# Kernel tuning notes

Hardware: AMD Instinct MI355X
Metric: run time of the kernel (lower is better)

## Reference

```python
import jax, jax.numpy as jnp
import numpy as np

B = 4096
D_FULL, D_T1, D_T2 = 1024, 512, 512
N_SPEC, N_SHARED = 4, 4
HID, OUT = 512, 256


def _expert_params(key, n_experts, d_in):
    k1, k2, k3, k4 = jax.random.split(key, 4)
    s1 = 1.0 / np.sqrt(d_in)
    s2 = 1.0 / np.sqrt(HID)
    return {
        'W1': jax.random.uniform(k1, (n_experts, d_in, HID), jnp.float32, -s1, s1),
        'b1': jax.random.uniform(k2, (n_experts, HID), jnp.float32, -s1, s1),
        'W2': jax.random.uniform(k3, (n_experts, HID, OUT), jnp.float32, -s2, s2),
        'b2': jax.random.uniform(k4, (n_experts, OUT), jnp.float32, -s2, s2),
    }


def setup_inputs() -> dict:
    key = jax.random.key(0)
    ks = jax.random.split(key, 12)
    x_full = jax.random.normal(ks[0], (B, D_FULL), jnp.float32)
    x_task1 = jax.random.normal(ks[1], (B, D_T1), jnp.float32)
    x_task2 = jax.random.normal(ks[2], (B, D_T2), jnp.float32)
    ps = _expert_params(ks[3], N_SHARED, D_FULL)
    p1 = _expert_params(ks[4], N_SPEC, D_T1)
    p2 = _expert_params(ks[5], N_SPEC, D_T2)
    sg = 1.0 / np.sqrt(D_FULL)
    s1 = 1.0 / np.sqrt(D_T1)
    s2 = 1.0 / np.sqrt(D_T2)
    return {
        'x_full': x_full, 'x_task1': x_task1, 'x_task2': x_task2,
        'sh_W1': ps['W1'], 'sh_b1': ps['b1'], 'sh_W2': ps['W2'], 'sh_b2': ps['b2'],
        't1_W1': p1['W1'], 't1_b1': p1['b1'], 't1_W2': p1['W2'], 't1_b2': p1['b2'],
        't2_W1': p2['W1'], 't2_b1': p2['b1'], 't2_W2': p2['W2'], 't2_b2': p2['b2'],
        'gsh_W': jax.random.uniform(ks[6], (D_FULL, 2 * N_SPEC + N_SHARED), jnp.float32, -sg, sg),
        'gsh_b': jax.random.uniform(ks[7], (2 * N_SPEC + N_SHARED,), jnp.float32, -sg, sg),
        'g1_W': jax.random.uniform(ks[8], (D_T1, N_SPEC + N_SHARED), jnp.float32, -s1, s1),
        'g1_b': jax.random.uniform(ks[9], (N_SPEC + N_SHARED,), jnp.float32, -s1, s1),
        'g2_W': jax.random.uniform(ks[10], (D_T2, N_SPEC + N_SHARED), jnp.float32, -s2, s2),
        'g2_b': jax.random.uniform(ks[11], (N_SPEC + N_SHARED,), jnp.float32, -s2, s2),
    }


def _experts(x, W1, b1, W2, b2):
    # x: [B, D]; W1: [E, D, H] -> out [E, B, OUT]
    h = jax.nn.relu(jnp.einsum('bd,edh->ebh', x, W1) + b1[:, None, :])
    return jax.nn.relu(jnp.einsum('ebh,eho->ebo', h, W2) + b2[:, None, :])


def reference(x_full, x_task1, x_task2,
              sh_W1, sh_b1, sh_W2, sh_b2,
              t1_W1, t1_b1, t1_W2, t1_b2,
              t2_W1, t2_b1, t2_W2, t2_b2,
              gsh_W, gsh_b, g1_W, g1_b, g2_W, g2_b):
    eo_shared = _experts(x_full, sh_W1, sh_b1, sh_W2, sh_b2)    # [Es, B, OUT]
    eo_t1 = _experts(x_task1, t1_W1, t1_b1, t1_W2, t1_b2)       # [Et, B, OUT]
    eo_t2 = _experts(x_task2, t2_W1, t2_b1, t2_W2, t2_b2)       # [Et, B, OUT]

    g1 = jax.nn.softmax(x_task1 @ g1_W + g1_b, axis=1)          # [B, Et+Es]
    out1 = jnp.einsum('ebc,be->bc', jnp.concatenate([eo_t1, eo_shared], axis=0), g1)

    g2 = jax.nn.softmax(x_task2 @ g2_W + g2_b, axis=1)
    out2 = jnp.einsum('ebc,be->bc', jnp.concatenate([eo_t2, eo_shared], axis=0), g2)

    gsh = jax.nn.softmax(x_full @ gsh_W + gsh_b, axis=1)        # [B, 2Et+Es]
    out_sh = jnp.einsum('ebc,be->bc', jnp.concatenate([eo_t1, eo_t2, eo_shared], axis=0), gsh)

    return (out_sh, out1, out2)
```

## Files before the change

kernel.cpp:

```cpp
#include <hip/hip_runtime.h>

typedef unsigned short u16;
typedef __attribute__((ext_vector_type(8))) short short8;
typedef __attribute__((ext_vector_type(4))) float f32x4;

#define GL2LDS16(src, dst) __builtin_amdgcn_global_load_lds( \
    (const __attribute__((address_space(1))) void*)(src),    \
    (__attribute__((address_space(3))) void*)(dst), 16, 0, 0)

__device__ __forceinline__ u16 f2bf(float f) {
  union { float f; unsigned u; } v; v.f = f;
  unsigned r = v.u + 0x7fffu + ((v.u >> 16) & 1u);
  return (u16)(r >> 16);
}
__device__ __forceinline__ float bf2f(u16 h) {
  union { unsigned u; float f; } v; v.u = ((unsigned)h) << 16; return v.f;
}

__global__ void k_cvt_bf16(const float* __restrict__ in, u16* __restrict__ out, int n8) {
  int i = blockIdx.x * 256 + threadIdx.x;
  if (i >= n8) return;
  const float4* p = (const float4*)in + 2 * (size_t)i;
  float4 a = p[0], b = p[1];
  short8 o;
  o[0] = (short)f2bf(a.x); o[1] = (short)f2bf(a.y); o[2] = (short)f2bf(a.z); o[3] = (short)f2bf(a.w);
  o[4] = (short)f2bf(b.x); o[5] = (short)f2bf(b.y); o[6] = (short)f2bf(b.z); o[7] = (short)f2bf(b.w);
  ((short8*)out)[i] = o;
}

__global__ void k_transpose_cvt(const float* __restrict__ in, u16* __restrict__ out, int R, int C) {
  __shared__ float tile[32][33];
  size_t zoff = (size_t)blockIdx.z * R * C;
  in += zoff; out += zoff;
  int c0 = blockIdx.x * 32, r0 = blockIdx.y * 32;
  int tx = threadIdx.x, ty = threadIdx.y;
#pragma unroll
  for (int i = ty; i < 32; i += 8)
    tile[i][tx] = in[(size_t)(r0 + i) * C + (c0 + tx)];
  __syncthreads();
#pragma unroll
  for (int i = ty; i < 32; i += 8)
    out[(size_t)(c0 + i) * R + (r0 + tx)] = f2bf(tile[tx][i]);
}

template <int NG, int KD>
__device__ __forceinline__ void gate_row(const float* __restrict__ x, const float* __restrict__ W,
                                         const float* __restrict__ bv, float* __restrict__ out,
                                         int b, int lane) {
  float s[NG];
#pragma unroll
  for (int j = 0; j < NG; ++j) s[j] = 0.f;
  const float* xr = x + (size_t)b * KD;
  for (int k = lane; k < KD; k += 64) {
    float xv = xr[k];
    const float* wr = W + (size_t)k * NG;
#pragma unroll
    for (int j = 0; j < NG; ++j) s[j] += xv * wr[j];
  }
#pragma unroll
  for (int off = 32; off >= 1; off >>= 1) {
#pragma unroll
    for (int j = 0; j < NG; ++j) s[j] += __shfl_xor(s[j], off, 64);
  }
#pragma unroll
  for (int j = 0; j < NG; ++j) s[j] += bv[j];
  float m = s[0];
#pragma unroll
  for (int j = 1; j < NG; ++j) m = fmaxf(m, s[j]);
  float tot = 0.f;
#pragma unroll
  for (int j = 0; j < NG; ++j) { s[j] = __expf(s[j] - m); tot += s[j]; }
  float inv = 1.f / tot;
  if (lane == 0) {
#pragma unroll
    for (int j = 0; j < NG; ++j) out[(size_t)b * NG + j] = s[j] * inv;
  }
}

__global__ void k_gates(const float* __restrict__ xf, const float* __restrict__ x1,
                        const float* __restrict__ x2,
                        const float* __restrict__ gshW, const float* __restrict__ gshB,
                        const float* __restrict__ g1W, const float* __restrict__ g1B,
                        const float* __restrict__ g2W, const float* __restrict__ g2B,
                        float* __restrict__ gsh, float* __restrict__ g1, float* __restrict__ g2) {
  int b = blockIdx.x, lane = threadIdx.x;
  gate_row<12, 1024>(xf, gshW, gshB, gsh, b, lane);
  gate_row<8, 512>(x1, g1W, g1B, g1, b, lane);
  gate_row<8, 512>(x2, g2W, g2B, g2, b, lane);
}

struct GemmDesc {
  const u16* A;
  const u16* BT;
  const float* bias;
  u16* C;
  int K;
  int N;
};
struct GemmArgs { GemmDesc d[12]; };

__global__ __launch_bounds__(256, 2) void k_gemm(GemmArgs args) {
  GemmDesc g = args.d[blockIdx.y];
  const int K = g.K, N = g.N;
  const int row0 = (blockIdx.x & 31) << 7;
  const int col0 = (blockIdx.x >> 5) << 7;

  __shared__ __align__(16) u16 As[128 * 32];
  __shared__ __align__(16) u16 Bs[128 * 32];

  const int lane = threadIdx.x & 63;
  const int wave = threadIdx.x >> 6;
  const int wr = (wave >> 1) << 6;
  const int wc = (wave & 1) << 6;
  const int lrow = lane & 15;
  const int kgrp = (lane >> 4) << 3;

  f32x4 acc[4][4];
#pragma unroll
  for (int m = 0; m < 4; ++m)
#pragma unroll
    for (int n = 0; n < 4; ++n)
      acc[m][n] = (f32x4){0.f, 0.f, 0.f, 0.f};

  for (int k0 = 0; k0 < K; k0 += 32) {
#pragma unroll
    for (int i = 0; i < 2; ++i) {
      const int cb = (i * 4 + wave) * 64;
      const int c = cb + lane;
      const int r = c >> 2;
      const int kk = (c & 3) << 3;
      GL2LDS16(g.A + (size_t)(row0 + r) * K + (k0 + kk), &As[cb * 8]);
      GL2LDS16(g.BT + (size_t)(col0 + r) * K + (k0 + kk), &Bs[cb * 8]);
    }
    __syncthreads();

    short8 a[4], b[4];
#pragma unroll
    for (int m = 0; m < 4; ++m)
      a[m] = *(const short8*)&As[(wr + (m << 4) + lrow) * 32 + kgrp];
#pragma unroll
    for (int n = 0; n < 4; ++n)
      b[n] = *(const short8*)&Bs[(wc + (n << 4) + lrow) * 32 + kgrp];
#pragma unroll
    for (int m = 0; m < 4; ++m)
#pragma unroll
      for (int n = 0; n < 4; ++n)
        acc[m][n] = __builtin_amdgcn_mfma_f32_16x16x32_bf16(a[m], b[n], acc[m][n], 0, 0, 0);
    __syncthreads();
  }

  const int rbase = (lane >> 4) << 2;
#pragma unroll
  for (int n = 0; n < 4; ++n) {
    const int gc = col0 + wc + (n << 4) + lrow;
    const float bv = g.bias[gc];
#pragma unroll
    for (int m = 0; m < 4; ++m) {
      const int gr = row0 + wr + (m << 4) + rbase;
#pragma unroll
      for (int j = 0; j < 4; ++j) {
        float o = acc[m][n][j] + bv;
        o = fmaxf(o, 0.f);
        g.C[(size_t)(gr + j) * N + gc] = f2bf(o);
      }
    }
  }
}

__global__ void k_reduce(const u16* __restrict__ OutB, const float* __restrict__ gsh,
                         const float* __restrict__ g1, const float* __restrict__ g2,
                         float* __restrict__ out) {
  int t = blockIdx.x * 256 + threadIdx.x;
  int b = t >> 5;
  int c0 = (t & 31) << 3;
  float wsh[12], w1[8], w2[8];
#pragma unroll
  for (int j = 0; j < 12; ++j) wsh[j] = gsh[(size_t)b * 12 + j];
#pragma unroll
  for (int j = 0; j < 8; ++j) { w1[j] = g1[(size_t)b * 8 + j]; w2[j] = g2[(size_t)b * 8 + j]; }
  float ash[8] = {0, 0, 0, 0, 0, 0, 0, 0};
  float a1[8] = {0, 0, 0, 0, 0, 0, 0, 0};
  float a2[8] = {0, 0, 0, 0, 0, 0, 0, 0};
#pragma unroll
  for (int e = 0; e < 12; ++e) {
    short8 v = *(const short8*)&OutB[((size_t)e * 4096 + b) * 256 + c0];
    float f[8];
#pragma unroll
    for (int i = 0; i < 8; ++i) f[i] = bf2f((u16)v[i]);
#pragma unroll
    for (int i = 0; i < 8; ++i) ash[i] += wsh[e] * f[i];
    if (e < 4) {
#pragma unroll
      for (int i = 0; i < 8; ++i) a1[i] += w1[e] * f[i];
    } else if (e < 8) {
#pragma unroll
      for (int i = 0; i < 8; ++i) a2[i] += w2[e - 4] * f[i];
    } else {
#pragma unroll
      for (int i = 0; i < 8; ++i) a1[i] += w1[e - 4] * f[i];
#pragma unroll
      for (int i = 0; i < 8; ++i) a2[i] += w2[e - 4] * f[i];
    }
  }
  size_t base = (size_t)b * 256 + c0;
  float4* o;
  o = (float4*)(out + base);
  o[0] = make_float4(ash[0], ash[1], ash[2], ash[3]);
  o[1] = make_float4(ash[4], ash[5], ash[6], ash[7]);
  o = (float4*)(out + 4096ull * 256 + base);
  o[0] = make_float4(a1[0], a1[1], a1[2], a1[3]);
  o[1] = make_float4(a1[4], a1[5], a1[6], a1[7]);
  o = (float4*)(out + 2ull * 4096 * 256 + base);
  o[0] = make_float4(a2[0], a2[1], a2[2], a2[3]);
  o[1] = make_float4(a2[4], a2[5], a2[6], a2[7]);
}

extern "C" void kernel_launch(void* const* d_in, const int* in_sizes, int n_in,
                              void* d_out, int out_size, void* d_ws, size_t ws_size,
                              hipStream_t stream) {
  const float* x_full = (const float*)d_in[0];
  const float* x_t1 = (const float*)d_in[1];
  const float* x_t2 = (const float*)d_in[2];
  const float* sh_W1 = (const float*)d_in[3];
  const float* sh_b1 = (const float*)d_in[4];
  const float* sh_W2 = (const float*)d_in[5];
  const float* sh_b2 = (const float*)d_in[6];
  const float* t1_W1 = (const float*)d_in[7];
  const float* t1_b1 = (const float*)d_in[8];
  const float* t1_W2 = (const float*)d_in[9];
  const float* t1_b2 = (const float*)d_in[10];
  const float* t2_W1 = (const float*)d_in[11];
  const float* t2_b1 = (const float*)d_in[12];
  const float* t2_W2 = (const float*)d_in[13];
  const float* t2_b2 = (const float*)d_in[14];
  const float* gsh_W = (const float*)d_in[15];
  const float* gsh_b = (const float*)d_in[16];
  const float* g1_W = (const float*)d_in[17];
  const float* g1_b = (const float*)d_in[18];
  const float* g2_W = (const float*)d_in[19];
  const float* g2_b = (const float*)d_in[20];

  char* ws = (char*)d_ws;
  size_t off = 0;
  auto alloc = [&](size_t bytes) -> void* {
    void* p = ws + off;
    off += (bytes + 255) & ~(size_t)255;
    return p;
  };
  u16* xf_b = (u16*)alloc(4096ull * 1024 * 2);
  u16* x1_b = (u16*)alloc(4096ull * 512 * 2);
  u16* x2_b = (u16*)alloc(4096ull * 512 * 2);
  u16* w1t_t1 = (u16*)alloc(4ull * 512 * 512 * 2);
  u16* w1t_t2 = (u16*)alloc(4ull * 512 * 512 * 2);
  u16* w1t_sh = (u16*)alloc(4ull * 512 * 1024 * 2);
  u16* w2t = (u16*)alloc(12ull * 256 * 512 * 2);
  u16* H = (u16*)alloc(12ull * 4096 * 512 * 2);
  u16* OutB = (u16*)alloc(12ull * 4096 * 256 * 2);
  float* gshv = (float*)alloc(4096ull * 12 * 4);
  float* g1v = (float*)alloc(4096ull * 8 * 4);
  float* g2v = (float*)alloc(4096ull * 8 * 4);

  k_cvt_bf16<<<4096 * 1024 / 8 / 256, 256, 0, stream>>>(x_full, xf_b, 4096 * 1024 / 8);
  k_cvt_bf16<<<4096 * 512 / 8 / 256, 256, 0, stream>>>(x_t1, x1_b, 4096 * 512 / 8);
  k_cvt_bf16<<<4096 * 512 / 8 / 256, 256, 0, stream>>>(x_t2, x2_b, 4096 * 512 / 8);

  k_transpose_cvt<<<dim3(16, 16, 4), dim3(32, 8), 0, stream>>>(t1_W1, w1t_t1, 512, 512);
  k_transpose_cvt<<<dim3(16, 16, 4), dim3(32, 8), 0, stream>>>(t2_W1, w1t_t2, 512, 512);
  k_transpose_cvt<<<dim3(16, 32, 4), dim3(32, 8), 0, stream>>>(sh_W1, w1t_sh, 1024, 512);
  k_transpose_cvt<<<dim3(8, 16, 4), dim3(32, 8), 0, stream>>>(t1_W2, w2t, 512, 256);
  k_transpose_cvt<<<dim3(8, 16, 4), dim3(32, 8), 0, stream>>>(t2_W2, w2t + 4ull * 256 * 512, 512, 256);
  k_transpose_cvt<<<dim3(8, 16, 4), dim3(32, 8), 0, stream>>>(sh_W2, w2t + 8ull * 256 * 512, 512, 256);

  k_gates<<<4096, 64, 0, stream>>>(x_full, x_t1, x_t2, gsh_W, gsh_b, g1_W, g1_b, g2_W, g2_b,
                                   gshv, g1v, g2v);

  GemmArgs ga1;
  for (int e = 0; e < 4; ++e) {
    ga1.d[e] = GemmDesc{xf_b, w1t_sh + (size_t)e * 512 * 1024, sh_b1 + e * 512,
                        H + (size_t)(8 + e) * 4096 * 512, 1024, 512};
    ga1.d[4 + e] = GemmDesc{x1_b, w1t_t1 + (size_t)e * 512 * 512, t1_b1 + e * 512,
                            H + (size_t)e * 4096 * 512, 512, 512};
    ga1.d[8 + e] = GemmDesc{x2_b, w1t_t2 + (size_t)e * 512 * 512, t2_b1 + e * 512,
                            H + (size_t)(4 + e) * 4096 * 512, 512, 512};
  }
  k_gemm<<<dim3(128, 12), 256, 0, stream>>>(ga1);

  GemmArgs ga2;
  for (int e = 0; e < 12; ++e) {
    const float* bias = (e < 4) ? (t1_b2 + e * 256)
                      : (e < 8) ? (t2_b2 + (e - 4) * 256)
                                : (sh_b2 + (e - 8) * 256);
    ga2.d[e] = GemmDesc{H + (size_t)e * 4096 * 512, w2t + (size_t)e * 256 * 512, bias,
                        OutB + (size_t)e * 4096 * 256, 512, 256};
  }
  k_gemm<<<dim3(64, 12), 256, 0, stream>>>(ga2);

  k_reduce<<<512, 256, 0, stream>>>(OutB, gshv, g1v, g2v, (float*)d_out);
}
```

Measured before the change: 131.1 us.

## Pipeline GEMM with triple-buffered swizzled LDS, fuse conversion into gates, batch transposes

The GEMM now uses 256x128 tiles with 8 waves, BK=64, and a three-stage LDS ring fed by global_load_lds with XOR swizzling to avoid bank conflicts. Loads for step t+2 are interleaved with MFMA work, and s_setprio raises priority around the MFMA blocks. The bf16 input conversion is folded into the gate kernel, and the six weight transposes are merged into one launch, which cuts launch count and reads of x. In exchange the GEMM uses much more LDS per block and hand-tuned waitcnt and barrier sequencing that is harder to get right.

After: 117.9 us. 1.11x faster.

```diff
diff --git a/kernel.cpp b/kernel.cpp
--- a/kernel.cpp
+++ b/kernel.cpp
@@ -17,76 +17,108 @@
   union { unsigned u; float f; } v; v.u = ((unsigned)h) << 16; return v.f;
 }
 
-__global__ void k_cvt_bf16(const float* __restrict__ in, u16* __restrict__ out, int n8) {
-  int i = blockIdx.x * 256 + threadIdx.x;
-  if (i >= n8) return;
-  const float4* p = (const float4*)in + 2 * (size_t)i;
-  float4 a = p[0], b = p[1];
-  short8 o;
-  o[0] = (short)f2bf(a.x); o[1] = (short)f2bf(a.y); o[2] = (short)f2bf(a.z); o[3] = (short)f2bf(a.w);
-  o[4] = (short)f2bf(b.x); o[5] = (short)f2bf(b.y); o[6] = (short)f2bf(b.z); o[7] = (short)f2bf(b.w);
-  ((short8*)out)[i] = o;
-}
-
-__global__ void k_transpose_cvt(const float* __restrict__ in, u16* __restrict__ out, int R, int C) {
+__global__ void k_gates_cvt(const float* __restrict__ xf, const float* __restrict__ x1,
+                            const float* __restrict__ x2,
+                            const float* __restrict__ gshW, const float* __restrict__ gshB,
+                            const float* __restrict__ g1W, const float* __restrict__ g1B,
+                            const float* __restrict__ g2W, const float* __restrict__ g2B,
+                            u16* __restrict__ xfb, u16* __restrict__ x1b, u16* __restrict__ x2b,
+                            float* __restrict__ gsh, float* __restrict__ g1o,
+                            float* __restrict__ g2o) {
+  const int b = blockIdx.x, lane = threadIdx.x;
+  float s[12];
+#pragma unroll
+  for (int j = 0; j < 12; ++j) s[j] = 0.f;
+  {
+    const float* xr = xf + (size_t)b * 1024;
+    u16* xw = xfb + (size_t)b * 1024;
+    for (int k = lane; k < 1024; k += 64) {
+      float v = xr[k];
+      xw[k] = f2bf(v);
+      const float* wr = gshW + (size_t)k * 12;
+#pragma unroll
+      for (int j = 0; j < 12; ++j) s[j] += v * wr[j];
+    }
+  }
+  float u[8], w[8];
+#pragma unroll
+  for (int j = 0; j < 8; ++j) { u[j] = 0.f; w[j] = 0.f; }
+  {
+    const float* xr1 = x1 + (size_t)b * 512;
+    const float* xr2 = x2 + (size_t)b * 512;
+    u16* xw1 = x1b + (size_t)b * 512;
+    u16* xw2 = x2b + (size_t)b * 512;
+    for (int k = lane; k < 512; k += 64) {
+      float v1 = xr1[k], v2 = xr2[k];
+      xw1[k] = f2bf(v1); xw2[k] = f2bf(v2);
+      const float* w1r = g1W + (size_t)k * 8;
+      const float* w2r = g2W + (size_t)k * 8;
+#pragma unroll
+      for (int j = 0; j < 8; ++j) { u[j] += v1 * w1r[j]; w[j] += v2 * w2r[j]; }
+    }
+  }
+#pragma unroll
+  for (int off = 32; off >= 1; off >>= 1) {
+#pragma unroll
+    for (int j = 0; j < 12; ++j) s[j] += __shfl_xor(s[j], off, 64);
+#pragma unroll
+    for (int j = 0; j < 8; ++j) { u[j] += __shfl_xor(u[j], off, 64); w[j] += __shfl_xor(w[j], off, 64); }
+  }
+  if (lane == 0) {
+    float m = -1e30f, tot = 0.f;
+#pragma unroll
+    for (int j = 0; j < 12; ++j) { s[j] += gshB[j]; m = fmaxf(m, s[j]); }
+#pragma unroll
+    for (int j = 0; j < 12; ++j) { s[j] = __expf(s[j] - m); tot += s[j]; }
+    float inv = 1.f / tot;
+#pragma unroll
+    for (int j = 0; j < 12; ++j) gsh[(size_t)b * 12 + j] = s[j] * inv;
+    m = -1e30f; tot = 0.f;
+#pragma unroll
+    for (int j = 0; j < 8; ++j) { u[j] += g1B[j]; m = fmaxf(m, u[j]); }
+#pragma unroll
+    for (int j = 0; j < 8; ++j) { u[j] = __expf(u[j] - m); tot += u[j]; }
+    inv = 1.f / tot;
+#pragma unroll
+    for (int j = 0; j < 8; ++j) g1o[(size_t)b * 8 + j] = u[j] * inv;
+    m = -1e30f; tot = 0.f;
+#pragma unroll
+    for (int j = 0; j < 8; ++j) { w[j] += g2B[j]; m = fmaxf(m, w[j]); }
+#pragma unroll
+    for (int j = 0; j < 8; ++j) { w[j] = __expf(w[j] - m); tot += w[j]; }
+    inv = 1.f / tot;
+#pragma unroll
+    for (int j = 0; j < 8; ++j) g2o[(size_t)b * 8 + j] = w[j] * inv;
+  }
+}
+
+struct TD { const float* src; u16* dst; int lgTps; int lgNtx; int R; int C; int tileBase; };
+struct TArgs { TD d[6]; };
+
+__global__ void k_transpose_all(TArgs ta) {
   __shared__ float tile[32][33];
-  size_t zoff = (size_t)blockIdx.z * R * C;
-  in += zoff; out += zoff;
-  int c0 = blockIdx.x * 32, r0 = blockIdx.y * 32;
-  int tx = threadIdx.x, ty = threadIdx.y;
-#pragma unroll
-  for (int i = ty; i < 32; i += 8)
-    tile[i][tx] = in[(size_t)(r0 + i) * C + (c0 + tx)];
+  const int x = blockIdx.x;
+  int di = 0;
+#pragma unroll
+  for (int i = 1; i < 6; ++i)
+    if (x >= ta.d[i].tileBase) di = i;
+  TD d = ta.d[di];
+  const int local = x - d.tileBase;
+  const int slice = local >> d.lgTps;
+  const int ti = local & ((1 << d.lgTps) - 1);
+  const int tx = ti & ((1 << d.lgNtx) - 1);
+  const int ty = ti >> d.lgNtx;
+  const float* src = d.src + (size_t)slice * d.R * d.C;
+  u16* dst = d.dst + (size_t)slice * d.R * d.C;
+  const int c0 = tx * 32, r0 = ty * 32;
+  const int ttx = threadIdx.x, tty = threadIdx.y;
+#pragma unroll
+  for (int i = tty; i < 32; i += 8)
+    tile[i][ttx] = src[(size_t)(r0 + i) * d.C + (c0 + ttx)];
   __syncthreads();
 #pragma unroll
-  for (int i = ty; i < 32; i += 8)
-    out[(size_t)(c0 + i) * R + (r0 + tx)] = f2bf(tile[tx][i]);
-}
-
-template <int NG, int KD>
-__device__ __forceinline__ void gate_row(const float* __restrict__ x, const float* __restrict__ W,
-                                         const float* __restrict__ bv, float* __restrict__ out,
-                                         int b, int lane) {
-  float s[NG];
-#pragma unroll
-  for (int j = 0; j < NG; ++j) s[j] = 0.f;
-  const float* xr = x + (size_t)b * KD;
-  for (int k = lane; k < KD; k += 64) {
-    float xv = xr[k];
-    const float* wr = W + (size_t)k * NG;
-#pragma unroll
-    for (int j = 0; j < NG; ++j) s[j] += xv * wr[j];
-  }
-#pragma unroll
-  for (int off = 32; off >= 1; off >>= 1) {
-#pragma unroll
-    for (int j = 0; j < NG; ++j) s[j] += __shfl_xor(s[j], off, 64);
-  }
-#pragma unroll
-  for (int j = 0; j < NG; ++j) s[j] += bv[j];
-  float m = s[0];
-#pragma unroll
-  for (int j = 1; j < NG; ++j) m = fmaxf(m, s[j]);
-  float tot = 0.f;
-#pragma unroll
-  for (int j = 0; j < NG; ++j) { s[j] = __expf(s[j] - m); tot += s[j]; }
-  float inv = 1.f / tot;
-  if (lane == 0) {
-#pragma unroll
-    for (int j = 0; j < NG; ++j) out[(size_t)b * NG + j] = s[j] * inv;
-  }
-}
-
-__global__ void k_gates(const float* __restrict__ xf, const float* __restrict__ x1,
-                        const float* __restrict__ x2,
-                        const float* __restrict__ gshW, const float* __restrict__ gshB,
-                        const float* __restrict__ g1W, const float* __restrict__ g1B,
-                        const float* __restrict__ g2W, const float* __restrict__ g2B,
-                        float* __restrict__ gsh, float* __restrict__ g1, float* __restrict__ g2) {
-  int b = blockIdx.x, lane = threadIdx.x;
-  gate_row<12, 1024>(xf, gshW, gshB, gsh, b, lane);
-  gate_row<8, 512>(x1, g1W, g1B, g1, b, lane);
-  gate_row<8, 512>(x2, g2W, g2B, g2, b, lane);
+  for (int i = tty; i < 32; i += 8)
+    dst[(size_t)(c0 + i) * d.R + (r0 + ttx)] = f2bf(tile[ttx][i]);
 }
 
 struct GemmDesc {
@@ -99,21 +131,51 @@
 };
 struct GemmArgs { GemmDesc d[12]; };
 
-__global__ __launch_bounds__(256, 2) void k_gemm(GemmArgs args) {
+__global__ __launch_bounds__(512) void k_gemm8(GemmArgs args) {
+  __shared__ __align__(16) u16 As[3 * 16384];
+  __shared__ __align__(16) u16 Bs[3 * 8192];
+
   GemmDesc g = args.d[blockIdx.y];
   const int K = g.K, N = g.N;
-  const int row0 = (blockIdx.x & 31) << 7;
-  const int col0 = (blockIdx.x >> 5) << 7;
-
-  __shared__ __align__(16) u16 As[128 * 32];
-  __shared__ __align__(16) u16 Bs[128 * 32];
-
-  const int lane = threadIdx.x & 63;
-  const int wave = threadIdx.x >> 6;
-  const int wr = (wave >> 1) << 6;
-  const int wc = (wave & 1) << 6;
+  const int ntN = N >> 7;
+  const int lg = (ntN == 4) ? 2 : 1;
+  const int bx = blockIdx.x;
+  const int row0 = (bx >> lg) << 8;
+  const int col0 = (bx & (ntN - 1)) << 7;
+
+  const int tid = threadIdx.x;
+  const int lane = tid & 63;
+  const int wid = tid >> 6;
+  const int wm = wid >> 1;
+  const int wn = wid & 1;
   const int lrow = lane & 15;
-  const int kgrp = (lane >> 4) << 3;
+  const int lkq = lane >> 4;
+  const int sw = lrow & 7;
+  const int cx0 = lkq ^ sw;
+  const int cx1 = (4 | lkq) ^ sw;
+
+  int aoffs[4], boffs[4];
+#pragma unroll
+  for (int m = 0; m < 4; ++m) aoffs[m] = ((wm << 6) + (m << 4) + lrow) << 3;
+#pragma unroll
+  for (int n = 0; n < 4; ++n) boffs[n] = ((wn << 6) + (n << 4) + lrow) << 3;
+
+  auto stageA = [&](int s, int kt, int j) {
+    const int cb = (j << 9) + (wid << 6);
+    const int c = cb + lane;
+    const int r = c >> 3;
+    const int gch = (c & 7) ^ (r & 7);
+    GL2LDS16(g.A + (size_t)(row0 + r) * K + (kt << 6) + (gch << 3),
+             &As[s * 16384 + cb * 8]);
+  };
+  auto stageB = [&](int s, int kt, int j) {
+    const int cb = (j << 9) + (wid << 6);
+    const int c = cb + lane;
+    const int r = c >> 3;
+    const int gch = (c & 7) ^ (r & 7);
+    GL2LDS16(g.BT + (size_t)(col0 + r) * K + (kt << 6) + (gch << 3),
+             &Bs[s * 8192 + cb * 8]);
+  };
 
   f32x4 acc[4][4];
 #pragma unroll
@@ -122,45 +184,74 @@
     for (int n = 0; n < 4; ++n)
       acc[m][n] = (f32x4){0.f, 0.f, 0.f, 0.f};
 
-  for (int k0 = 0; k0 < K; k0 += 32) {
-#pragma unroll
-    for (int i = 0; i < 2; ++i) {
-      const int cb = (i * 4 + wave) * 64;
-      const int c = cb + lane;
-      const int r = c >> 2;
-      const int kk = (c & 3) << 3;
-      GL2LDS16(g.A + (size_t)(row0 + r) * K + (k0 + kk), &As[cb * 8]);
-      GL2LDS16(g.BT + (size_t)(col0 + r) * K + (k0 + kk), &Bs[cb * 8]);
-    }
-    __syncthreads();
-
+  const int T = K >> 6;
+#pragma unroll
+  for (int j = 0; j < 4; ++j) stageA(0, 0, j);
+#pragma unroll
+  for (int j = 0; j < 2; ++j) stageB(0, 0, j);
+#pragma unroll
+  for (int j = 0; j < 4; ++j) stageA(1, 1, j);
+#pragma unroll
+  for (int j = 0; j < 2; ++j) stageB(1, 1, j);
+  asm volatile("s_waitcnt vmcnt(6)" ::: "memory");
+  __builtin_amdgcn_s_barrier();
+
+  int slot = 0;
+  for (int t = 0; t < T; ++t) {
+    const u16* Asl = &As[slot * 16384];
+    const u16* Bsl = &Bs[slot * 8192];
+    const int s2 = (slot >= 1) ? slot - 1 : 2;
     short8 a[4], b[4];
-#pragma unroll
-    for (int m = 0; m < 4; ++m)
-      a[m] = *(const short8*)&As[(wr + (m << 4) + lrow) * 32 + kgrp];
-#pragma unroll
-    for (int n = 0; n < 4; ++n)
-      b[n] = *(const short8*)&Bs[(wc + (n << 4) + lrow) * 32 + kgrp];
+
+#pragma unroll
+    for (int m = 0; m < 4; ++m) a[m] = *(const short8*)&Asl[(aoffs[m] | cx0) << 3];
+#pragma unroll
+    for (int n = 0; n < 4; ++n) b[n] = *(const short8*)&Bsl[(boffs[n] | cx0) << 3];
+    if (t + 2 < T) { stageA(s2, t + 2, 0); stageA(s2, t + 2, 1); stageB(s2, t + 2, 0); }
+    __builtin_amdgcn_s_barrier();
+    asm volatile("s_waitcnt lgkmcnt(0)" ::: "memory");
+    __builtin_amdgcn_sched_barrier(0);
+    __builtin_amdgcn_s_setprio(1);
 #pragma unroll
     for (int m = 0; m < 4; ++m)
 #pragma unroll
       for (int n = 0; n < 4; ++n)
         acc[m][n] = __builtin_amdgcn_mfma_f32_16x16x32_bf16(a[m], b[n], acc[m][n], 0, 0, 0);
-    __syncthreads();
-  }
-
-  const int rbase = (lane >> 4) << 2;
+    __builtin_amdgcn_s_setprio(0);
+    __builtin_amdgcn_s_barrier();
+
+#pragma unroll
+    for (int m = 0; m < 4; ++m) a[m] = *(const short8*)&Asl[(aoffs[m] | cx1) << 3];
+#pragma unroll
+    for (int n = 0; n < 4; ++n) b[n] = *(const short8*)&Bsl[(boffs[n] | cx1) << 3];
+    if (t + 2 < T) { stageA(s2, t + 2, 2); stageA(s2, t + 2, 3); stageB(s2, t + 2, 1); }
+    __builtin_amdgcn_s_barrier();
+    asm volatile("s_waitcnt lgkmcnt(0)" ::: "memory");
+    __builtin_amdgcn_sched_barrier(0);
+    __builtin_amdgcn_s_setprio(1);
+#pragma unroll
+    for (int m = 0; m < 4; ++m)
+#pragma unroll
+      for (int n = 0; n < 4; ++n)
+        acc[m][n] = __builtin_amdgcn_mfma_f32_16x16x32_bf16(a[m], b[n], acc[m][n], 0, 0, 0);
+    __builtin_amdgcn_s_setprio(0);
+    asm volatile("s_waitcnt vmcnt(6)" ::: "memory");
+    __builtin_amdgcn_s_barrier();
+
+    slot = (slot == 2) ? 0 : slot + 1;
+  }
+
+  const int rb = lkq << 2;
 #pragma unroll
   for (int n = 0; n < 4; ++n) {
-    const int gc = col0 + wc + (n << 4) + lrow;
+    const int gc = col0 + (wn << 6) + (n << 4) + lrow;
     const float bv = g.bias[gc];
 #pragma unroll
     for (int m = 0; m < 4; ++m) {
-      const int gr = row0 + wr + (m << 4) + rbase;
+      const int gr = row0 + (wm << 6) + (m << 4) + rb;
 #pragma unroll
       for (int j = 0; j < 4; ++j) {
-        float o = acc[m][n][j] + bv;
-        o = fmaxf(o, 0.f);
+        float o = fmaxf(acc[m][n][j] + bv, 0.f);
         g.C[(size_t)(gr + j) * N + gc] = f2bf(o);
       }
     }
@@ -260,19 +351,17 @@
   float* g1v = (float*)alloc(4096ull * 8 * 4);
   float* g2v = (float*)alloc(4096ull * 8 * 4);
 
-  k_cvt_bf16<<<4096 * 1024 / 8 / 256, 256, 0, stream>>>(x_full, xf_b, 4096 * 1024 / 8);
-  k_cvt_bf16<<<4096 * 512 / 8 / 256, 256, 0, stream>>>(x_t1, x1_b, 4096 * 512 / 8);
-  k_cvt_bf16<<<4096 * 512 / 8 / 256, 256, 0, stream>>>(x_t2, x2_b, 4096 * 512 / 8);
-
-  k_transpose_cvt<<<dim3(16, 16, 4), dim3(32, 8), 0, stream>>>(t1_W1, w1t_t1, 512, 512);
-  k_transpose_cvt<<<dim3(16, 16, 4), dim3(32, 8), 0, stream>>>(t2_W1, w1t_t2, 512, 512);
-  k_transpose_cvt<<<dim3(16, 32, 4), dim3(32, 8), 0, stream>>>(sh_W1, w1t_sh, 1024, 512);
-  k_transpose_cvt<<<dim3(8, 16, 4), dim3(32, 8), 0, stream>>>(t1_W2, w2t, 512, 256);
-  k_transpose_cvt<<<dim3(8, 16, 4), dim3(32, 8), 0, stream>>>(t2_W2, w2t + 4ull * 256 * 512, 512, 256);
-  k_transpose_cvt<<<dim3(8, 16, 4), dim3(32, 8), 0, stream>>>(sh_W2, w2t + 8ull * 256 * 512, 512, 256);
-
-  k_gates<<<4096, 64, 0, stream>>>(x_full, x_t1, x_t2, gsh_W, gsh_b, g1_W, g1_b, g2_W, g2_b,
-                                   gshv, g1v, g2v);
+  k_gates_cvt<<<4096, 64, 0, stream>>>(x_full, x_t1, x_t2, gsh_W, gsh_b, g1_W, g1_b, g2_W, g2_b,
+                                       xf_b, x1_b, x2_b, gshv, g1v, g2v);
+
+  TArgs ta;
+  ta.d[0] = TD{t1_W1, w1t_t1, 8, 4, 512, 512, 0};
+  ta.d[1] = TD{t2_W1, w1t_t2, 8, 4, 512, 512, 1024};
+  ta.d[2] = TD{sh_W1, w1t_sh, 9, 4, 1024, 512, 2048};
+  ta.d[3] = TD{t1_W2, w2t, 7, 3, 512, 256, 4096};
+  ta.d[4] = TD{t2_W2, w2t + 4ull * 256 * 512, 7, 3, 512, 256, 4608};
+  ta.d[5] = TD{sh_W2, w2t + 8ull * 256 * 512, 7, 3, 512, 256, 5120};
+  k_transpose_all<<<5632, dim3(32, 8), 0, stream>>>(ta);
 
   GemmArgs ga1;
   for (int e = 0; e < 4; ++e) {
@@ -283,7 +372,7 @@
     ga1.d[8 + e] = GemmDesc{x2_b, w1t_t2 + (size_t)e * 512 * 512, t2_b1 + e * 512,
                             H + (size_t)(4 + e) * 4096 * 512, 512, 512};
   }
-  k_gemm<<<dim3(128, 12), 256, 0, stream>>>(ga1);
+  k_gemm8<<<dim3(64, 12), 512, 0, stream>>>(ga1);
 
   GemmArgs ga2;
   for (int e = 0; e < 12; ++e) {
@@ -293,7 +382,7 @@
     ga2.d[e] = GemmDesc{H + (size_t)e * 4096 * 512, w2t + (size_t)e * 256 * 512, bias,
                         OutB + (size_t)e * 4096 * 256, 512, 256};
   }
-  k_gemm<<<dim3(64, 12), 256, 0, stream>>>(ga2);
+  k_gemm8<<<dim3(32, 12), 512, 0, stream>>>(ga2);
 
   k_reduce<<<512, 256, 0, stream>>>(OutB, gshv, g1v, g2v, (float*)d_out);
 }
```
